# Kernel optimization log

Measured on AMD Instinct MI355X. Metric: run time of the kernel, lower is better.

Reference implementation:

```python
import jax, jax.numpy as jnp
import numpy as np

N_EMBD = 1024
N_HEAD = 16
HEAD_DIM = N_EMBD // N_HEAD


def setup_inputs() -> dict:
    key = jax.random.key(0)
    k1, k2, k3, k4, k5 = jax.random.split(key, 5)
    x = jax.random.normal(k1, (4, 2048, N_EMBD), dtype=jnp.float32)
    s_in = 1.0 / np.sqrt(N_EMBD)
    W_attn = jax.random.normal(k2, (N_EMBD, 3 * N_EMBD), dtype=jnp.float32) * s_in
    b_attn = jax.random.normal(k3, (3 * N_EMBD,), dtype=jnp.float32) * 0.01
    W_proj = jax.random.normal(k4, (N_EMBD, N_EMBD), dtype=jnp.float32) * s_in
    b_proj = jax.random.normal(k5, (N_EMBD,), dtype=jnp.float32) * 0.01
    return {"x": x, "W_attn": W_attn, "b_attn": b_attn, "W_proj": W_proj, "b_proj": b_proj}


def reference(x, W_attn, b_attn, W_proj, b_proj):
    B, T, C = x.shape
    qkv = jnp.einsum('btc,cd->btd', x, W_attn) + b_attn  # [B,T,3C]
    q, k, v = jnp.split(qkv, 3, axis=2)
    # [B,T,C] -> [B,H,T,Dh]
    def heads(t):
        return t.reshape(B, T, N_HEAD, HEAD_DIM).transpose(0, 2, 1, 3)
    q, k, v = heads(q), heads(k), heads(v)
    scale = HEAD_DIM ** -0.5
    att = jnp.einsum('bhqd,bhkd->bhqk', q, k) * scale  # [B,H,T,T]
    causal = jnp.tril(jnp.ones((T, T), dtype=bool))
    att = jnp.where(causal[None, None], att, -jnp.inf)
    att = jax.nn.softmax(att, axis=-1)
    y = jnp.einsum('bhqk,bhkd->bhqd', att, v)  # [B,H,T,Dh]
    y = y.transpose(0, 2, 1, 3).reshape(B, T, C)
    y = jnp.einsum('btc,cd->btd', y, W_proj) + b_proj
    return y
```

## Files before the change

kernel.cpp:

```cpp
#include <hip/hip_runtime.h>

typedef unsigned short u16;
typedef unsigned int u32;
typedef __bf16 bf16x8 __attribute__((ext_vector_type(8)));
typedef u16 u16x8 __attribute__((ext_vector_type(8)));
typedef u16 u16x4 __attribute__((ext_vector_type(4)));
typedef float f32x4 __attribute__((ext_vector_type(4)));
typedef float f32x16 __attribute__((ext_vector_type(16)));

#define BHTD 8388608
#define QSCALE 0.18033688f
#define SMAX 16.0f

__device__ __forceinline__ u16 f2bf(float f) {
  union { float f; u32 u; } x; x.f = f;
  u32 r = (x.u + 0x7FFFu + ((x.u >> 16) & 1u)) >> 16;
  return (u16)r;
}

__device__ __forceinline__ u32 cvt_pk_bf16(float lo, float hi) {
  u32 r;
  asm("v_cvt_pk_bf16_f32 %0, %1, %2" : "=v"(r) : "v"(lo), "v"(hi));
  return r;
}

__device__ __forceinline__ void permlane32_swap(u32& x, u32& y) {
  asm("v_permlane32_swap_b32 %0, %1" : "+v"(x), "+v"(y));
}

__device__ __forceinline__ void async_copy16(const u16* gsrc, u16* ldst) {
  __builtin_amdgcn_global_load_lds(
      (const __attribute__((address_space(1))) void*)gsrc,
      (__attribute__((address_space(3))) void*)ldst, 16, 0, 0);
}

#define MF(a, b, c) __builtin_amdgcn_mfma_f32_16x16x32_bf16((a), (b), (c), 0, 0, 0)

__global__ __launch_bounds__(256) void conv_x_kernel(const float4* __restrict__ in,
                                                     u16x4* __restrict__ out, int n4) {
  int i = blockIdx.x * 256 + threadIdx.x;
  int stride = gridDim.x * 256;
  for (; i < n4; i += stride) {
    float4 v = in[i];
    u16x4 o = { f2bf(v.x), f2bf(v.y), f2bf(v.z), f2bf(v.w) };
    out[i] = o;
  }
}

__global__ __launch_bounds__(256) void transpose_bf16(const float* __restrict__ W,
                                                      u16* __restrict__ Wt, int K, int N) {
  __shared__ float t[64][65];
  int c0 = blockIdx.x * 64;
  int r0 = blockIdx.y * 64;
  int c = threadIdx.x & 63;
  int r4 = threadIdx.x >> 6;
#pragma unroll
  for (int j = 0; j < 16; ++j) {
    int r = j * 4 + r4;
    t[r][c] = W[(size_t)(r0 + r) * N + (c0 + c)];
  }
  __syncthreads();
#pragma unroll
  for (int j = 0; j < 16; ++j) {
    int n = j * 4 + r4;
    Wt[(size_t)(c0 + n) * K + (r0 + c)] = f2bf(t[c][n]);
  }
}

template <int MODE>
__global__ __launch_bounds__(512, 2) void gemm_bf16(const u16* __restrict__ A,
                                                    const u16* __restrict__ Bt,
                                                    const float* __restrict__ bias,
                                                    float* __restrict__ outp,
                                                    u16* __restrict__ qkv, int grid_n) {
  __shared__ __attribute__((aligned(16))) u16 Al[3][256 * 64];
  __shared__ __attribute__((aligned(16))) u16 Bl[3][128 * 64];
  const int tid = threadIdx.x;
  const int lane = tid & 63, wave = tid >> 6;
  const int wr = wave >> 1, wc = wave & 1;
  const int bn = blockIdx.x % grid_n, bm = blockIdx.x / grid_n;
  const int m0 = bm * 256, n0 = bn * 128;
  const int g = lane >> 4, c16 = lane & 15;
  const int xs = c16 & 7;
  const int offK0 = ((g ^ xs) << 3);
  const int offK1 = (((4 + g) ^ xs) << 3);

#define STAGE_A_(t, s, c)                                                         \
  {                                                                               \
    int row_ = (c) >> 3, sl_ = (c) & 7;                                           \
    async_copy16(&A[(size_t)(m0 + row_) * 1024 + (t) * 64 + ((sl_ ^ (row_ & 7)) << 3)], \
                 &Al[s][(c) << 3]);                                               \
  }
#define STAGE_B_(t, s, c)                                                         \
  {                                                                               \
    int row_ = (c) >> 3, sl_ = (c) & 7;                                           \
    async_copy16(&Bt[(size_t)(n0 + row_) * 1024 + (t) * 64 + ((sl_ ^ (row_ & 7)) << 3)], \
                 &Bl[s][(c) << 3]);                                               \
  }

  f32x4 acc[4][4] = {};
  bf16x8 aF[2][4][2], bF[2][4][2];

#pragma unroll
  for (int t = 0; t < 3; ++t) {
    STAGE_B_(t, t, tid); STAGE_B_(t, t, tid + 512);
    STAGE_A_(t, t, tid); STAGE_A_(t, t, tid + 512);
    STAGE_A_(t, t, tid + 1024); STAGE_A_(t, t, tid + 1536);
  }
  asm volatile("s_waitcnt vmcnt(12)" ::: "memory");
  __builtin_amdgcn_s_barrier();
#pragma unroll
  for (int m = 0; m < 4; ++m) {
    int row = wr * 64 + m * 16 + c16;
    aF[0][m][0] = *(const bf16x8*)&Al[0][row * 64 + offK0];
    aF[0][m][1] = *(const bf16x8*)&Al[0][row * 64 + offK1];
  }
#pragma unroll
  for (int n = 0; n < 4; ++n) {
    int row = wc * 64 + n * 16 + c16;
    bF[0][n][0] = *(const bf16x8*)&Bl[0][row * 64 + offK0];
    bF[0][n][1] = *(const bf16x8*)&Bl[0][row * 64 + offK1];
  }
  asm volatile("s_waitcnt lgkmcnt(0)" ::: "memory");
  __builtin_amdgcn_s_barrier();

#pragma unroll
  for (int j = 0; j < 16; ++j) {
    const int cur = j & 1, nxt = cur ^ 1;
    const int sR = (j + 1) % 3;
    const int sW = j % 3;
    const bool rd = (j < 15);
    const bool st = (j < 13);

    if (j <= 13) {
      asm volatile("s_waitcnt vmcnt(6)" ::: "memory");
    } else if (j == 14) {
      asm volatile("s_waitcnt vmcnt(0)" ::: "memory");
    }
    __builtin_amdgcn_s_barrier();

    if (rd) {
#pragma unroll
      for (int m = 0; m < 4; ++m) {
        int row = wr * 64 + m * 16 + c16;
        aF[nxt][m][0] = *(const bf16x8*)&Al[sR][row * 64 + offK0];
        aF[nxt][m][1] = *(const bf16x8*)&Al[sR][row * 64 + offK1];
      }
    }
    if (st) STAGE_B_(j + 3, sW, tid);
    __builtin_amdgcn_s_setprio(1);
#pragma unroll
    for (int n = 0; n < 4; ++n) acc[0][n] = MF(aF[cur][0][0], bF[cur][n][0], acc[0][n]);
#pragma unroll
    for (int n = 0; n < 4; ++n) acc[1][n] = MF(aF[cur][1][0], bF[cur][n][0], acc[1][n]);
    __builtin_amdgcn_s_setprio(0);
    __builtin_amdgcn_s_barrier();

    if (rd) {
#pragma unroll
      for (int n = 0; n < 4; ++n) {
        int row = wc * 64 + n * 16 + c16;
        bF[nxt][n][0] = *(const bf16x8*)&Bl[sR][row * 64 + offK0];
        bF[nxt][n][1] = *(const bf16x8*)&Bl[sR][row * 64 + offK1];
      }
    }
    if (st) STAGE_B_(j + 3, sW, tid + 512);
    __builtin_amdgcn_s_setprio(1);
#pragma unroll
    for (int n = 0; n < 4; ++n) acc[2][n] = MF(aF[cur][2][0], bF[cur][n][0], acc[2][n]);
#pragma unroll
    for (int n = 0; n < 4; ++n) acc[3][n] = MF(aF[cur][3][0], bF[cur][n][0], acc[3][n]);
    __builtin_amdgcn_s_setprio(0);
    __builtin_amdgcn_s_barrier();

    if (st) { STAGE_A_(j + 3, sW, tid); STAGE_A_(j + 3, sW, tid + 512); }
    __builtin_amdgcn_s_setprio(1);
#pragma unroll
    for (int n = 0; n < 4; ++n) acc[0][n] = MF(aF[cur][0][1], bF[cur][n][1], acc[0][n]);
#pragma unroll
    for (int n = 0; n < 4; ++n) acc[1][n] = MF(aF[cur][1][1], bF[cur][n][1], acc[1][n]);
    __builtin_amdgcn_s_setprio(0);
    __builtin_amdgcn_s_barrier();

    if (st) { STAGE_A_(j + 3, sW, tid + 1024); STAGE_A_(j + 3, sW, tid + 1536); }
    __builtin_amdgcn_s_setprio(1);
#pragma unroll
    for (int n = 0; n < 4; ++n) acc[2][n] = MF(aF[cur][2][1], bF[cur][n][1], acc[2][n]);
#pragma unroll
    for (int n = 0; n < 4; ++n) acc[3][n] = MF(aF[cur][3][1], bF[cur][n][1], acc[3][n]);
    __builtin_amdgcn_s_setprio(0);
    __builtin_amdgcn_s_barrier();
  }

  float bv[4];
#pragma unroll
  for (int nb = 0; nb < 4; ++nb) bv[nb] = bias[n0 + wc * 64 + nb * 16 + c16];

#pragma unroll
  for (int mb = 0; mb < 4; ++mb) {
    int row0 = m0 + wr * 64 + mb * 16 + g * 4;
#pragma unroll
    for (int nb = 0; nb < 4; ++nb) {
      int col = n0 + wc * 64 + nb * 16 + c16;
      float bvn = bv[nb];
      if (MODE == 0) {
        int sel = col >> 10, ci = col & 1023;
        int hh = ci >> 6, d = ci & 63;
        int bb = row0 >> 11, t0 = row0 & 2047;
        float qs = (sel == 0) ? QSCALE : 1.0f;
        if (sel == 2) {
          u16x4 pk;
#pragma unroll
          for (int r = 0; r < 4; ++r) pk[r] = f2bf(acc[mb][nb][r] + bvn);
          *(u16x4*)&qkv[(size_t)2 * BHTD + (((size_t)(bb * 16 + hh) * 64 + d) << 11) + t0] = pk;
        } else {
#pragma unroll
          for (int r = 0; r < 4; ++r) {
            qkv[(size_t)sel * BHTD + (((size_t)(bb * 16 + hh) * 2048 + t0 + r) << 6) + d] =
                f2bf((acc[mb][nb][r] + bvn) * qs);
          }
        }
      } else {
#pragma unroll
        for (int r = 0; r < 4; ++r)
          outp[((size_t)(row0 + r) << 10) + col] = acc[mb][nb][r] + bvn;
      }
    }
  }
#undef STAGE_A_
#undef STAGE_B_
}

__global__ __launch_bounds__(512, 4) void attn_fwd(const u16* __restrict__ Q,
                                                   const u16* __restrict__ K,
                                                   const u16* __restrict__ VT,
                                                   u16* __restrict__ Y) {
  __shared__ __attribute__((aligned(16))) u16 Kl[2][2][64 * 64];
  __shared__ __attribute__((aligned(16))) u16 Vl[2][2][64 * 64];
  float* Pl = (float*)&Kl[0][0][0];
  float* Ll = (float*)&Vl[0][0][0];
  const float NEG_BIG = -1e30f;

  int bid = blockIdx.x;
  int p = bid >> 6, hd = bid & 63;
  size_t hb = (size_t)hd * (2048 * 64);
  const u16* Qh = Q + hb;
  const u16* Kh = K + hb;
  const u16* Vh = VT + hb;
  int tid = threadIdx.x, lane = tid & 63, w = tid >> 6;
  int rg = w & 3, par = w >> 2;
  int c32 = lane & 31, h = lane >> 5;
  const int xs = c32 & 7;

  int srow = tid >> 3;
  int swz = ((tid & 7) ^ (srow & 7)) << 3;

  for (int pass = 0; pass < 2; ++pass) {
    const int t128 = pass ? p : (15 - p);
    const int iters = t128 + 1;
    const int qrow = t128 * 128 + rg * 32 + c32;

    bf16x8 qf[4];
#pragma unroll
    for (int dk = 0; dk < 4; ++dk)
      qf[dk] = *(const bf16x8*)&Qh[(size_t)qrow * 64 + dk * 16 + 8 * h];

    async_copy16(&Kh[(size_t)srow * 64 + swz], &Kl[0][0][tid << 3]);
    async_copy16(&Kh[(size_t)(64 + srow) * 64 + swz], &Kl[0][1][tid << 3]);
    async_copy16(&Vh[(size_t)srow * 2048 + swz], &Vl[0][0][tid << 3]);
    async_copy16(&Vh[(size_t)srow * 2048 + 64 + swz], &Vl[0][1][tid << 3]);

    float l = 0.f;
    f32x16 o0 = {}, o1 = {};

    for (int it = 0; it < iters; ++it) {
      int cb = it & 1;
      __syncthreads();

      if (it + 1 < iters) {
        int kve = (it + 1) << 7, kvo = kve + 64;
        async_copy16(&Kh[(size_t)(kve + srow) * 64 + swz], &Kl[cb ^ 1][0][tid << 3]);
        async_copy16(&Kh[(size_t)(kvo + srow) * 64 + swz], &Kl[cb ^ 1][1][tid << 3]);
        async_copy16(&Vh[(size_t)srow * 2048 + kve + swz], &Vl[cb ^ 1][0][tid << 3]);
        async_copy16(&Vh[(size_t)srow * 2048 + kvo + swz], &Vl[cb ^ 1][1][tid << 3]);
      }

      const bool lastit = (it + 1 == iters);
      if (par && lastit && rg < 2) continue;
      const int kv0 = (2 * it + par) << 6;
      const bool mask = lastit && ((par == 0) == (rg < 2));

      bf16x8 kf[2][4];
#pragma unroll
      for (int kb = 0; kb < 2; ++kb)
#pragma unroll
        for (int dk = 0; dk < 4; ++dk)
          kf[kb][dk] =
              *(const bf16x8*)&Kl[cb][par][(kb * 32 + c32) * 64 + (((2 * dk + h) ^ xs) << 3)];
      f32x16 s0, s1;
#pragma unroll
      for (int i = 0; i < 16; ++i) { s0[i] = -SMAX; s1[i] = -SMAX; }
      __builtin_amdgcn_s_setprio(1);
#pragma unroll
      for (int dk = 0; dk < 4; ++dk) {
        s0 = __builtin_amdgcn_mfma_f32_32x32x16_bf16(kf[0][dk], qf[dk], s0, 0, 0, 0);
        s1 = __builtin_amdgcn_mfma_f32_32x32x16_bf16(kf[1][dk], qf[dk], s1, 0, 0, 0);
      }
      __builtin_amdgcn_s_setprio(0);

      if (mask) {
        int kvb = kv0 + 4 * h;
#pragma unroll
        for (int reg = 0; reg < 16; ++reg) {
          int kvl = kvb + 8 * (reg >> 2) + (reg & 3);
          if (kvl > qrow) s0[reg] = NEG_BIG;
          if (kvl + 32 > qrow) s1[reg] = NEG_BIG;
        }
      }

#pragma unroll
      for (int i = 0; i < 16; ++i) s0[i] = __builtin_exp2f(s0[i]);
#pragma unroll
      for (int i = 0; i < 16; ++i) s1[i] = __builtin_exp2f(s1[i]);
      float b0 = s0[0] + s1[0], b1 = s0[1] + s1[1];
      float b2 = s0[2] + s1[2], b3 = s0[3] + s1[3];
#pragma unroll
      for (int i = 4; i < 16; i += 4) {
        b0 += s0[i] + s1[i];
        b1 += s0[i + 1] + s1[i + 1];
        b2 += s0[i + 2] + s1[i + 2];
        b3 += s0[i + 3] + s1[i + 3];
      }
      float rs = (b0 + b1) + (b2 + b3);
      rs += __shfl_xor(rs, 32);
      l += rs;

      u32 pw0[8], pw1[8];
#pragma unroll
      for (int mm = 0; mm < 8; ++mm) {
        pw0[mm] = cvt_pk_bf16(s0[2 * mm], s0[2 * mm + 1]);
        pw1[mm] = cvt_pk_bf16(s1[2 * mm], s1[2 * mm + 1]);
      }
      permlane32_swap(pw0[0], pw0[2]); permlane32_swap(pw0[1], pw0[3]);
      permlane32_swap(pw0[4], pw0[6]); permlane32_swap(pw0[5], pw0[7]);
      permlane32_swap(pw1[0], pw1[2]); permlane32_swap(pw1[1], pw1[3]);
      permlane32_swap(pw1[4], pw1[6]); permlane32_swap(pw1[5], pw1[7]);

      __builtin_amdgcn_s_setprio(1);
#pragma unroll
      for (int c = 0; c < 4; ++c) {
        const u32* pp = (c >> 1) ? pw1 : pw0;
        const int a = 4 * (c & 1);
        union { u32 u[4]; bf16x8 v; } pf;
        pf.u[0] = pp[a + 0];
        pf.u[1] = pp[a + 1];
        pf.u[2] = pp[a + 2];
        pf.u[3] = pp[a + 3];
        bf16x8 vfa = *(const bf16x8*)&Vl[cb][par][c32 * 64 + (((2 * c + h) ^ xs) << 3)];
        bf16x8 vfb = *(const bf16x8*)&Vl[cb][par][(32 + c32) * 64 + (((2 * c + h) ^ xs) << 3)];
        o0 = __builtin_amdgcn_mfma_f32_32x32x16_bf16(vfa, pf.v, o0, 0, 0, 0);
        o1 = __builtin_amdgcn_mfma_f32_32x32x16_bf16(vfb, pf.v, o1, 0, 0, 0);
      }
      __builtin_amdgcn_s_setprio(0);
    }

    __syncthreads();

    if (par == 1) {
#pragma unroll
      for (int db = 0; db < 2; ++db)
#pragma unroll
        for (int rq = 0; rq < 4; ++rq)
#pragma unroll
          for (int jj = 0; jj < 4; ++jj) {
            int d = db * 32 + 8 * rq + 4 * h + jj;
            Pl[rg * 2048 + d * 32 + c32] = (db ? o1[rq * 4 + jj] : o0[rq * 4 + jj]);
          }
      if (h == 0) Ll[rg * 32 + c32] = l;
    }
    __syncthreads();
    if (par == 0) {
      float lt = l + Ll[rg * 32 + c32];
      float inv = 1.0f / lt;
      size_t yb =
          (size_t)(hd >> 4) * (2048 * 1024) + (size_t)(hd & 15) * 64 + (size_t)qrow * 1024;
#pragma unroll
      for (int db = 0; db < 2; ++db)
#pragma unroll
        for (int rq = 0; rq < 4; ++rq) {
          u16x4 pk;
#pragma unroll
          for (int jj = 0; jj < 4; ++jj) {
            int d = db * 32 + 8 * rq + 4 * h + jj;
            float v = (db ? o1[rq * 4 + jj] : o0[rq * 4 + jj]) + Pl[rg * 2048 + d * 32 + c32];
            pk[jj] = f2bf(v * inv);
          }
          *(u16x4*)&Y[yb + db * 32 + 8 * rq + 4 * h] = pk;
        }
    }
    __syncthreads();
  }
}

extern "C" void kernel_launch(void* const* d_in, const int* in_sizes, int n_in,
                              void* d_out, int out_size, void* d_ws, size_t ws_size,
                              hipStream_t stream) {
  (void)in_sizes; (void)n_in; (void)out_size; (void)ws_size;
  const float* x      = (const float*)d_in[0];
  const float* W_attn = (const float*)d_in[1];
  const float* b_attn = (const float*)d_in[2];
  const float* W_proj = (const float*)d_in[3];
  const float* b_proj = (const float*)d_in[4];
  float* out = (float*)d_out;

  char* ws = (char*)d_ws;
  u16* Xb  = (u16*)(ws);
  u16* Wt  = (u16*)(ws + 16777216);
  u16* Wpt = (u16*)(ws + 16777216 + 6291456);
  u16* QKV = (u16*)(ws + 16777216 + 6291456 + 2097152);
  u16* Yb  = Xb;

  conv_x_kernel<<<2048, 256, 0, stream>>>((const float4*)x, (u16x4*)Xb, 2097152);
  transpose_bf16<<<dim3(48, 16), 256, 0, stream>>>(W_attn, Wt, 1024, 3072);
  transpose_bf16<<<dim3(16, 16), 256, 0, stream>>>(W_proj, Wpt, 1024, 1024);
  gemm_bf16<0><<<768, 512, 0, stream>>>(Xb, Wt, b_attn, nullptr, QKV, 24);
  attn_fwd<<<512, 512, 0, stream>>>(QKV, QKV + BHTD, QKV + 2 * BHTD, Yb);
  gemm_bf16<1><<<256, 512, 0, stream>>>(Yb, Wpt, b_proj, out, nullptr, 8);
}
```

Before: 175.6 us.

## Split causal attention into smaller 64-row blocks with single-buffered KV tiles

Each attention block now has 256 threads and handles one 64-row query tile over 64-key KV tiles, giving 2048 blocks instead of 512. The old paired-pass load balancing and double-buffered K/V shared memory are gone. K and V share one smaller buffer, which should allow higher occupancy and finer scheduling granularity across the GPU. The trade-off is that the next tile's async load is issued only after compute, so the compute/load overlap within a block is lost, and there are more per-block prologue and epilogue costs.

```diff
diff --git a/kernel.cpp b/kernel.cpp
--- a/kernel.cpp
+++ b/kernel.cpp
@@ -231,133 +231,97 @@
 #undef STAGE_B_
 }
 
-__global__ __launch_bounds__(512, 4) void attn_fwd(const u16* __restrict__ Q,
+__global__ __launch_bounds__(256, 8) void attn_fwd(const u16* __restrict__ Q,
                                                    const u16* __restrict__ K,
                                                    const u16* __restrict__ VT,
                                                    u16* __restrict__ Y) {
-  __shared__ __attribute__((aligned(16))) u16 Kl[2][2][64 * 64];
-  __shared__ __attribute__((aligned(16))) u16 Vl[2][2][64 * 64];
-  float* Pl = (float*)&Kl[0][0][0];
-  float* Ll = (float*)&Vl[0][0][0];
+  __shared__ __attribute__((aligned(16))) u16 KV[2][64 * 64];
+  __shared__ float Ll[64];
+  float* Pl = (float*)&KV[0][0];
   const float NEG_BIG = -1e30f;
 
   int bid = blockIdx.x;
-  int p = bid >> 6, hd = bid & 63;
+  int qt = bid >> 6, hd = bid & 63;
   size_t hb = (size_t)hd * (2048 * 64);
   const u16* Qh = Q + hb;
   const u16* Kh = K + hb;
   const u16* Vh = VT + hb;
   int tid = threadIdx.x, lane = tid & 63, w = tid >> 6;
-  int rg = w & 3, par = w >> 2;
+  int rg = w & 1, par = w >> 1;
   int c32 = lane & 31, h = lane >> 5;
   const int xs = c32 & 7;
-
-  int srow = tid >> 3;
-  int swz = ((tid & 7) ^ (srow & 7)) << 3;
-
-  for (int pass = 0; pass < 2; ++pass) {
-    const int t128 = pass ? p : (15 - p);
-    const int iters = t128 + 1;
-    const int qrow = t128 * 128 + rg * 32 + c32;
-
-    bf16x8 qf[4];
-#pragma unroll
-    for (int dk = 0; dk < 4; ++dk)
-      qf[dk] = *(const bf16x8*)&Qh[(size_t)qrow * 64 + dk * 16 + 8 * h];
-
-    async_copy16(&Kh[(size_t)srow * 64 + swz], &Kl[0][0][tid << 3]);
-    async_copy16(&Kh[(size_t)(64 + srow) * 64 + swz], &Kl[0][1][tid << 3]);
-    async_copy16(&Vh[(size_t)srow * 2048 + swz], &Vl[0][0][tid << 3]);
-    async_copy16(&Vh[(size_t)srow * 2048 + 64 + swz], &Vl[0][1][tid << 3]);
-
-    float l = 0.f;
-    f32x16 o0 = {}, o1 = {};
-
-    for (int it = 0; it < iters; ++it) {
-      int cb = it & 1;
-      __syncthreads();
-
-      if (it + 1 < iters) {
-        int kve = (it + 1) << 7, kvo = kve + 64;
-        async_copy16(&Kh[(size_t)(kve + srow) * 64 + swz], &Kl[cb ^ 1][0][tid << 3]);
-        async_copy16(&Kh[(size_t)(kvo + srow) * 64 + swz], &Kl[cb ^ 1][1][tid << 3]);
-        async_copy16(&Vh[(size_t)srow * 2048 + kve + swz], &Vl[cb ^ 1][0][tid << 3]);
-        async_copy16(&Vh[(size_t)srow * 2048 + kvo + swz], &Vl[cb ^ 1][1][tid << 3]);
-      }
-
-      const bool lastit = (it + 1 == iters);
-      if (par && lastit && rg < 2) continue;
-      const int kv0 = (2 * it + par) << 6;
-      const bool mask = lastit && ((par == 0) == (rg < 2));
-
-      bf16x8 kf[2][4];
-#pragma unroll
-      for (int kb = 0; kb < 2; ++kb)
-#pragma unroll
-        for (int dk = 0; dk < 4; ++dk)
-          kf[kb][dk] =
-              *(const bf16x8*)&Kl[cb][par][(kb * 32 + c32) * 64 + (((2 * dk + h) ^ xs) << 3)];
-      f32x16 s0, s1;
-#pragma unroll
-      for (int i = 0; i < 16; ++i) { s0[i] = -SMAX; s1[i] = -SMAX; }
+  const int qrow = qt * 64 + rg * 32 + c32;
+
+  int ch0 = tid, ch1 = tid + 256;
+  int sr0 = ch0 >> 3, sw0 = ((ch0 & 7) ^ (sr0 & 7)) << 3;
+  int sr1 = ch1 >> 3, sw1 = ((ch1 & 7) ^ (sr1 & 7)) << 3;
+
+  bf16x8 qf[4];
+#pragma unroll
+  for (int dk = 0; dk < 4; ++dk)
+    qf[dk] = *(const bf16x8*)&Qh[(size_t)qrow * 64 + dk * 16 + 8 * h];
+
+  async_copy16(&Kh[(size_t)sr0 * 64 + sw0], &KV[0][ch0 << 3]);
+  async_copy16(&Kh[(size_t)sr1 * 64 + sw1], &KV[0][ch1 << 3]);
+  async_copy16(&Vh[(size_t)sr0 * 2048 + sw0], &KV[1][ch0 << 3]);
+  async_copy16(&Vh[(size_t)sr1 * 2048 + sw1], &KV[1][ch1 << 3]);
+
+  float l = 0.f;
+  f32x16 o0 = {}, o1 = {};
+
+  for (int it = 0; it <= qt; ++it) {
+    __syncthreads();
+
+    const bool lastit = (it == qt);
+    if (!(lastit && rg == 0 && par == 1)) {
+      const int kv0 = (it << 6) + par * 32;
+
+      bf16x8 kf[4];
+#pragma unroll
+      for (int dk = 0; dk < 4; ++dk)
+        kf[dk] = *(const bf16x8*)&KV[0][(par * 32 + c32) * 64 + (((2 * dk + h) ^ xs) << 3)];
+      f32x16 s0;
+#pragma unroll
+      for (int i = 0; i < 16; ++i) s0[i] = -SMAX;
       __builtin_amdgcn_s_setprio(1);
 #pragma unroll
-      for (int dk = 0; dk < 4; ++dk) {
-        s0 = __builtin_amdgcn_mfma_f32_32x32x16_bf16(kf[0][dk], qf[dk], s0, 0, 0, 0);
-        s1 = __builtin_amdgcn_mfma_f32_32x32x16_bf16(kf[1][dk], qf[dk], s1, 0, 0, 0);
-      }
+      for (int dk = 0; dk < 4; ++dk)
+        s0 = __builtin_amdgcn_mfma_f32_32x32x16_bf16(kf[dk], qf[dk], s0, 0, 0, 0);
       __builtin_amdgcn_s_setprio(0);
 
-      if (mask) {
+      if (lastit) {
         int kvb = kv0 + 4 * h;
 #pragma unroll
         for (int reg = 0; reg < 16; ++reg) {
           int kvl = kvb + 8 * (reg >> 2) + (reg & 3);
           if (kvl > qrow) s0[reg] = NEG_BIG;
-          if (kvl + 32 > qrow) s1[reg] = NEG_BIG;
         }
       }
 
 #pragma unroll
       for (int i = 0; i < 16; ++i) s0[i] = __builtin_exp2f(s0[i]);
-#pragma unroll
-      for (int i = 0; i < 16; ++i) s1[i] = __builtin_exp2f(s1[i]);
-      float b0 = s0[0] + s1[0], b1 = s0[1] + s1[1];
-      float b2 = s0[2] + s1[2], b3 = s0[3] + s1[3];
-#pragma unroll
-      for (int i = 4; i < 16; i += 4) {
-        b0 += s0[i] + s1[i];
-        b1 += s0[i + 1] + s1[i + 1];
-        b2 += s0[i + 2] + s1[i + 2];
-        b3 += s0[i + 3] + s1[i + 3];
-      }
+      float b0 = s0[0] + s0[4], b1 = s0[1] + s0[5], b2 = s0[2] + s0[6], b3 = s0[3] + s0[7];
+      b0 += s0[8] + s0[12]; b1 += s0[9] + s0[13]; b2 += s0[10] + s0[14]; b3 += s0[11] + s0[15];
       float rs = (b0 + b1) + (b2 + b3);
       rs += __shfl_xor(rs, 32);
       l += rs;
 
-      u32 pw0[8], pw1[8];
-#pragma unroll
-      for (int mm = 0; mm < 8; ++mm) {
-        pw0[mm] = cvt_pk_bf16(s0[2 * mm], s0[2 * mm + 1]);
-        pw1[mm] = cvt_pk_bf16(s1[2 * mm], s1[2 * mm + 1]);
-      }
+      u32 pw0[8];
+#pragma unroll
+      for (int mm = 0; mm < 8; ++mm) pw0[mm] = cvt_pk_bf16(s0[2 * mm], s0[2 * mm + 1]);
       permlane32_swap(pw0[0], pw0[2]); permlane32_swap(pw0[1], pw0[3]);
       permlane32_swap(pw0[4], pw0[6]); permlane32_swap(pw0[5], pw0[7]);
-      permlane32_swap(pw1[0], pw1[2]); permlane32_swap(pw1[1], pw1[3]);
-      permlane32_swap(pw1[4], pw1[6]); permlane32_swap(pw1[5], pw1[7]);
 
       __builtin_amdgcn_s_setprio(1);
 #pragma unroll
-      for (int c = 0; c < 4; ++c) {
-        const u32* pp = (c >> 1) ? pw1 : pw0;
-        const int a = 4 * (c & 1);
+      for (int c = 0; c < 2; ++c) {
+        const int a = 4 * c;
         union { u32 u[4]; bf16x8 v; } pf;
-        pf.u[0] = pp[a + 0];
-        pf.u[1] = pp[a + 1];
-        pf.u[2] = pp[a + 2];
-        pf.u[3] = pp[a + 3];
-        bf16x8 vfa = *(const bf16x8*)&Vl[cb][par][c32 * 64 + (((2 * c + h) ^ xs) << 3)];
-        bf16x8 vfb = *(const bf16x8*)&Vl[cb][par][(32 + c32) * 64 + (((2 * c + h) ^ xs) << 3)];
+        pf.u[0] = pw0[a + 0]; pf.u[1] = pw0[a + 1];
+        pf.u[2] = pw0[a + 2]; pf.u[3] = pw0[a + 3];
+        int slot = ((4 * par + 2 * c + h) ^ xs) << 3;
+        bf16x8 vfa = *(const bf16x8*)&KV[1][c32 * 64 + slot];
+        bf16x8 vfb = *(const bf16x8*)&KV[1][(32 + c32) * 64 + slot];
         o0 = __builtin_amdgcn_mfma_f32_32x32x16_bf16(vfa, pf.v, o0, 0, 0, 0);
         o1 = __builtin_amdgcn_mfma_f32_32x32x16_bf16(vfb, pf.v, o1, 0, 0, 0);
       }
@@ -366,39 +330,46 @@
 
     __syncthreads();
 
-    if (par == 1) {
-#pragma unroll
-      for (int db = 0; db < 2; ++db)
-#pragma unroll
-        for (int rq = 0; rq < 4; ++rq)
-#pragma unroll
-          for (int jj = 0; jj < 4; ++jj) {
-            int d = db * 32 + 8 * rq + 4 * h + jj;
-            Pl[rg * 2048 + d * 32 + c32] = (db ? o1[rq * 4 + jj] : o0[rq * 4 + jj]);
-          }
-      if (h == 0) Ll[rg * 32 + c32] = l;
-    }
-    __syncthreads();
-    if (par == 0) {
-      float lt = l + Ll[rg * 32 + c32];
-      float inv = 1.0f / lt;
-      size_t yb =
-          (size_t)(hd >> 4) * (2048 * 1024) + (size_t)(hd & 15) * 64 + (size_t)qrow * 1024;
-#pragma unroll
-      for (int db = 0; db < 2; ++db)
-#pragma unroll
-        for (int rq = 0; rq < 4; ++rq) {
-          u16x4 pk;
-#pragma unroll
-          for (int jj = 0; jj < 4; ++jj) {
-            int d = db * 32 + 8 * rq + 4 * h + jj;
-            float v = (db ? o1[rq * 4 + jj] : o0[rq * 4 + jj]) + Pl[rg * 2048 + d * 32 + c32];
-            pk[jj] = f2bf(v * inv);
-          }
-          *(u16x4*)&Y[yb + db * 32 + 8 * rq + 4 * h] = pk;
+    if (it < qt) {
+      int kv1 = (it + 1) << 6;
+      async_copy16(&Kh[(size_t)(kv1 + sr0) * 64 + sw0], &KV[0][ch0 << 3]);
+      async_copy16(&Kh[(size_t)(kv1 + sr1) * 64 + sw1], &KV[0][ch1 << 3]);
+      async_copy16(&Vh[(size_t)sr0 * 2048 + kv1 + sw0], &KV[1][ch0 << 3]);
+      async_copy16(&Vh[(size_t)sr1 * 2048 + kv1 + sw1], &KV[1][ch1 << 3]);
+    }
+  }
+
+  if (par == 1) {
+#pragma unroll
+    for (int db = 0; db < 2; ++db)
+#pragma unroll
+      for (int rq = 0; rq < 4; ++rq)
+#pragma unroll
+        for (int jj = 0; jj < 4; ++jj) {
+          int d = db * 32 + 8 * rq + 4 * h + jj;
+          Pl[rg * 2048 + d * 32 + c32] = (db ? o1[rq * 4 + jj] : o0[rq * 4 + jj]);
         }
-    }
-    __syncthreads();
+    if (h == 0) Ll[rg * 32 + c32] = l;
+  }
+  __syncthreads();
+  if (par == 0) {
+    float lt = l + Ll[rg * 32 + c32];
+    float inv = 1.0f / lt;
+    size_t yb =
+        (size_t)(hd >> 4) * (2048 * 1024) + (size_t)(hd & 15) * 64 + (size_t)qrow * 1024;
+#pragma unroll
+    for (int db = 0; db < 2; ++db)
+#pragma unroll
+      for (int rq = 0; rq < 4; ++rq) {
+        u16x4 pk;
+#pragma unroll
+        for (int jj = 0; jj < 4; ++jj) {
+          int d = db * 32 + 8 * rq + 4 * h + jj;
+          float v = (db ? o1[rq * 4 + jj] : o0[rq * 4 + jj]) + Pl[rg * 2048 + d * 32 + c32];
+          pk[jj] = f2bf(v * inv);
+        }
+        *(u16x4*)&Y[yb + db * 32 + 8 * rq + 4 * h] = pk;
+      }
   }
 }
 
@@ -424,6 +395,6 @@
   transpose_bf16<<<dim3(48, 16), 256, 0, stream>>>(W_attn, Wt, 1024, 3072);
   transpose_bf16<<<dim3(16, 16), 256, 0, stream>>>(W_proj, Wpt, 1024, 1024);
   gemm_bf16<0><<<768, 512, 0, stream>>>(Xb, Wt, b_attn, nullptr, QKV, 24);
-  attn_fwd<<<512, 512, 0, stream>>>(QKV, QKV + BHTD, QKV + 2 * BHTD, Yb);
+  attn_fwd<<<2048, 256, 0, stream>>>(QKV, QKV + BHTD, QKV + 2 * BHTD, Yb);
   gemm_bf16<1><<<256, 512, 0, stream>>>(Yb, Wpt, b_proj, out, nullptr, 8);
 }
```

After: 481.8 us. 2.74x slower.
